# Optimization experiments

Measured on AMD Instinct MI355X. Metric: run time of the kernel, lower is better.

## Reference

```python
import jax, jax.numpy as jnp
import numpy as np

RES = (128, 128)       # frequency modes (fx, fy)
T = (1.0, 1.0)         # period per dimension
J = 2                  # simplex dimension (polygon)
B = 2                  # batch size
NV = 512               # num vertices = num elements (polygon ring)


def setup_inputs() -> dict:
    key = jax.random.key(0)
    V = jax.random.uniform(key, (B, NV, 2), dtype=jnp.float32)
    idx = jnp.arange(NV, dtype=jnp.int32)
    # polygon ring connectivity: edge i = (i, i+1 mod NV)
    E = jnp.broadcast_to(jnp.stack([idx, (idx + 1) % NV], axis=-1)[None], (B, NV, 2))
    D = jnp.ones((B, NV, 1), jnp.float32)
    return {"V": V, "E": E, "D": D}


def _omega():
    # freq_init='fft': integer fft/rfft frequencies, scaled by 2*pi/t per dim
    f0 = np.fft.fftfreq(RES[0], d=1.0 / RES[0])
    f1 = np.fft.rfftfreq(RES[1], d=1.0 / RES[1])
    om = np.stack(np.meshgrid(f0, f1, indexing='ij'), axis=-1).astype(np.float32)
    om[..., 0] *= 2.0 * np.pi / T[0]
    om[..., 1] *= 2.0 * np.pi / T[1]
    return jnp.asarray(om)  # (fx, fy//2+1, 2)


def reference(V, E, D):
    b, nv, nd = V.shape
    # subdim: append auxiliary origin vertex, turn edges into triangles
    Vaux = jnp.concatenate([V, jnp.zeros((b, 1, nd), V.dtype)], axis=1)
    Eaux = jnp.concatenate([E, jnp.full((b, E.shape[1], 1), nv, E.dtype)], axis=-1)
    P = jax.vmap(lambda v, e: v[e])(Vaux, Eaux)           # (B, ne, j+1, 2)
    # C = j! * signed simplex content = det of edge vectors (2x2)
    Vs = P[:, :, :J, :] - P[:, :, J:J + 1, :]
    C = (Vs[:, :, 0, 0] * Vs[:, :, 1, 1] - Vs[:, :, 0, 1] * Vs[:, :, 1, 0])[..., None]  # (B, ne, 1)
    omega = _omega()
    sig = jnp.einsum('bejd,xyd->bejxy', P, omega)         # (B, ne, 3, fx, fy2)
    esig = jnp.stack([jnp.cos(sig), -jnp.sin(sig)], axis=-1)  # (B, ne, 3, fx, fy2, 2)
    # divided-difference denominator: prod over circular shifts 1..j
    d1 = sig - sig[:, :, jnp.array([1, 2, 0])]
    d2 = sig - sig[:, :, jnp.array([2, 0, 1])]
    denom = d1 * d2
    zero = denom == 0
    tmp = jnp.sum(esig / jnp.where(zero, 1.0, denom)[..., None], axis=2)  # (B, ne, fx, fy2, 2)
    tmp = jnp.where(jnp.any(zero, axis=2)[..., None], 0.0, tmp)
    CD = C * D                                            # (B, ne, nch=1)
    F = jnp.einsum('bexyr,bec->bxycr', tmp, CD)           # (B, fx, fy2, 1, 2)
    # DC component: -1/j! * sum(C*D)
    dc = -jnp.sum(CD, axis=1) / 2.0                       # (B, 1)
    F = F.at[:, 0, 0].set(dc[..., None])
    F = -F                                                # img(F, deg=j=2): multiply by i^2 = -1
    F = F * (RES[0] ** J)                                 # density-preserving normalization
    return F
```

## Files before the change

kernel.cpp:

```cpp
#include <hip/hip_runtime.h>
#include <math.h>


#define NVERT 512
#define RESX  128
#define RESY2 65
#define BATCH 2
#define KXSPL 64
#define CHUNKS 8
#define ELEN  (NVERT / CHUNKS)

__device__ __forceinline__ float sig_eval(float x, float omx, float y, float omy) {
#pragma clang fp contract(off)
  float p = x * omx;
  float q = y * omy;
  return p + q;
}

extern "C" __global__ __launch_bounds__(512, 2)
void ddsl_spec(const float* __restrict__ V, const float* __restrict__ D,
               float* __restrict__ out) {
  const int lane = threadIdx.x;
  const int c    = threadIdx.y;
  const int ky   = blockIdx.x;
  const int b    = blockIdx.y;
  const int z    = blockIdx.z;

  __shared__ float2 sV[NVERT];
  __shared__ float  sCD[NVERT];
  __shared__ float  red[2][CHUNKS][KXSPL];
  __shared__ float  sDCv;

  const int tid = c * KXSPL + lane;

  {
    const float2* Vb = (const float2*)(V + b * (NVERT * 2));
    const int i = tid;
    const int j = (i + 1) & (NVERT - 1);
    float2 v0 = Vb[i];
    float2 v1 = Vb[j];
    float dv = D[b * NVERT + i];
    sV[i] = v0;
    sCD[i] = (v0.x * v1.y - v0.y * v1.x) * dv;
  }
  __syncthreads();

  const int kx = z * KXSPL + lane;
  const int kxi = (kx < 64) ? kx : kx - 128;
  const float kxf = (float)kxi;
  const float kyf = (float)ky;
  const float TWO_PI = 6.2831854820251465f;
  const float omx = TWO_PI * kxf;
  const float omy = TWO_PI * kyf;

  const int e0 = c * ELEN;

  float2 v = sV[e0];
  float s0 = sig_eval(v.x, omx, v.y, omy);
  float r0 = kxf * v.x + kyf * v.y;
  float rf0 = __builtin_amdgcn_fractf(r0);
  float c0  = __builtin_amdgcn_cosf(rf0);
  float sn0 = __builtin_amdgcn_sinf(rf0);

  float accRe = 0.0f, accIm = 0.0f;

#pragma unroll 4
  for (int e = e0; e < e0 + ELEN; ++e) {
    const int j = (e + 1) & (NVERT - 1);
    float2 v1 = sV[j];
    float cd = sCD[e];

    float s1 = sig_eval(v1.x, omx, v1.y, omy);
    float r1 = kxf * v1.x + kyf * v1.y;
    float rf1 = __builtin_amdgcn_fractf(r1);
    float c1  = __builtin_amdgcn_cosf(rf1);
    float sn1 = __builtin_amdgcn_sinf(rf1);

    float d01 = s0 - s1;
    float prod = s0 * s1 * d01;
    bool invalid = fabsf(prod) < 1e-30f;
    float cdE = invalid ? 0.0f : cd;
    float pr  = invalid ? 1.0f : prod;
    float inv = __builtin_amdgcn_rcpf(pr);

    float a0 = s1 * inv;
    float a1 = s0 * inv;
    float a2 = d01 * inv;
    float re = fmaf(c0, a0, fmaf(-c1, a1, a2));
    float im = fmaf(sn1, a1, -(sn0 * a0));

    accRe = fmaf(cdE, re, accRe);
    accIm = fmaf(cdE, im, accIm);

    s0 = s1; c0 = c1; sn0 = sn1;
  }

  red[0][c][lane] = accRe;
  red[1][c][lane] = accIm;
  __syncthreads();

  float val = 0.0f;
  if (c < 2) {
    float s = 0.0f;
#pragma unroll
    for (int k = 0; k < CHUNKS; ++k) s += red[c][k][lane];
    val = -16384.0f * s;
  } else if (c == 2 && ky == 0 && z == 0) {
    float s = 0.0f;
#pragma unroll
    for (int k = 0; k < NVERT / 64; ++k) s += sCD[lane + 64 * k];
    for (int off = 32; off > 0; off >>= 1) s += __shfl_down(s, off, 64);
    if (lane == 0) sDCv = 8192.0f * s;
  }
  __syncthreads();

  if (c < 2) {
    if (ky == 0 && z == 0 && lane == 0) val = sDCv;
    out[b * (RESX * RESY2 * 2) + kx * (RESY2 * 2) + ky * 2 + c] = val;
  }
}

extern "C" void kernel_launch(void* const* d_in, const int* in_sizes, int n_in,
                              void* d_out, int out_size, void* d_ws, size_t ws_size,
                              hipStream_t stream) {
  (void)in_sizes; (void)n_in; (void)d_ws; (void)ws_size; (void)out_size;
  const float* V = (const float*)d_in[0];
  const float* D = (const float*)d_in[2];
  float* out = (float*)d_out;

  dim3 grid(RESY2, BATCH, 2);
  dim3 block(KXSPL, CHUNKS, 1);
  ddsl_spec<<<grid, block, 0, stream>>>(V, D, out);
}
```

Measured before the change: 68.77 us.

## Repartition kx/edge work into smaller blocks and vectorize edge loop in pairs

Changes the block shape from 64 kx by 8 edge chunks to 16 kx by 16 edge chunks, and raises the grid depth from 2 to 8, so there are more, smaller blocks (256 threads) to spread over the GPU. The edge loop processes two edges per iteration with float2 vector types so the compiler can emit packed FP32 math. Vertices are stored as separate x and y arrays in shared memory. The phase is computed from sig times 1/(2π) instead of a separate dot product, which drops one multiply-add but can change rounding slightly. The risk is that smaller wave groups mean lanes in a wavefront read different edges, which could cause LDS bank conflicts, and each vertex block is reloaded by more blocks.

Measured after the change: 63.77 us. -7.3%, faster.

```diff
diff --git a/kernel.cpp b/kernel.cpp
--- a/kernel.cpp
+++ b/kernel.cpp
@@ -6,106 +6,118 @@
 #define RESX  128
 #define RESY2 65
 #define BATCH 2
-#define KXSPL 64
-#define CHUNKS 8
-#define ELEN  (NVERT / CHUNKS)
+#define NKX   16
+#define NCH   16
+#define ELEN  (NVERT / NCH)
 
-__device__ __forceinline__ float sig_eval(float x, float omx, float y, float omy) {
+typedef float f2 __attribute__((ext_vector_type(2)));
+
+__device__ __forceinline__ float sig1(float x, float y, float omx, float omy) {
 #pragma clang fp contract(off)
   float p = x * omx;
   float q = y * omy;
   return p + q;
 }
 
-extern "C" __global__ __launch_bounds__(512, 2)
+__device__ __forceinline__ f2 sig2(f2 x, f2 y, float omx, float omy) {
+#pragma clang fp contract(off)
+  f2 p = x * omx;
+  f2 q = y * omy;
+  return p + q;
+}
+
+extern "C" __global__ __launch_bounds__(256, 4)
 void ddsl_spec(const float* __restrict__ V, const float* __restrict__ D,
                float* __restrict__ out) {
-  const int lane = threadIdx.x;
-  const int c    = threadIdx.y;
-  const int ky   = blockIdx.x;
-  const int b    = blockIdx.y;
-  const int z    = blockIdx.z;
+  const int tx = threadIdx.x;
+  const int ty = threadIdx.y;
+  const int ky = blockIdx.x;
+  const int b  = blockIdx.y;
+  const int z  = blockIdx.z;
 
-  __shared__ float2 sV[NVERT];
-  __shared__ float  sCD[NVERT];
-  __shared__ float  red[2][CHUNKS][KXSPL];
-  __shared__ float  sDCv;
+  __shared__ float sVx[NVERT];
+  __shared__ float sVy[NVERT];
+  __shared__ __align__(8) float sCD[NVERT];
+  __shared__ float red[2][NCH][NKX];
+  __shared__ float sDCv;
 
-  const int tid = c * KXSPL + lane;
+  const int tid = ty * NKX + tx;
 
   {
     const float2* Vb = (const float2*)(V + b * (NVERT * 2));
-    const int i = tid;
-    const int j = (i + 1) & (NVERT - 1);
-    float2 v0 = Vb[i];
-    float2 v1 = Vb[j];
-    float dv = D[b * NVERT + i];
-    sV[i] = v0;
-    sCD[i] = (v0.x * v1.y - v0.y * v1.x) * dv;
+    for (int i = tid; i < NVERT; i += 256) {
+      const int j = (i + 1) & (NVERT - 1);
+      float2 v0 = Vb[i];
+      float2 v1 = Vb[j];
+      sVx[i] = v0.x;
+      sVy[i] = v0.y;
+      sCD[i] = (v0.x * v1.y - v0.y * v1.x) * D[b * NVERT + i];
+    }
   }
   __syncthreads();
 
-  const int kx = z * KXSPL + lane;
-  const int kxi = (kx < 64) ? kx : kx - 128;
-  const float kxf = (float)kxi;
+  const int kx = z * NKX + tx;
+  const float kxf = (float)((kx < 64) ? kx : kx - 128);
   const float kyf = (float)ky;
   const float TWO_PI = 6.2831854820251465f;
+  const float INV2PI = 0.15915493667125702f;
   const float omx = TWO_PI * kxf;
   const float omy = TWO_PI * kyf;
 
-  const int e0 = c * ELEN;
+  const int e0 = ty * ELEN;
 
-  float2 v = sV[e0];
-  float s0 = sig_eval(v.x, omx, v.y, omy);
-  float r0 = kxf * v.x + kyf * v.y;
-  float rf0 = __builtin_amdgcn_fractf(r0);
-  float c0  = __builtin_amdgcn_cosf(rf0);
-  float sn0 = __builtin_amdgcn_sinf(rf0);
+  float sP = sig1(sVx[e0], sVy[e0], omx, omy);
+  float rfP = __builtin_amdgcn_fractf(sP * INV2PI);
+  float cP  = __builtin_amdgcn_cosf(rfP);
+  float snP = __builtin_amdgcn_sinf(rfP);
 
-  float accRe = 0.0f, accIm = 0.0f;
+  f2 accRe = {0.0f, 0.0f};
+  f2 accIm = {0.0f, 0.0f};
 
 #pragma unroll 4
-  for (int e = e0; e < e0 + ELEN; ++e) {
-    const int j = (e + 1) & (NVERT - 1);
-    float2 v1 = sV[j];
-    float cd = sCD[e];
+  for (int t = 0; t < ELEN / 2; ++t) {
+    const int e = e0 + 2 * t;
+    const int j1 = (e + 1) & (NVERT - 1);
+    const int j2 = (e + 2) & (NVERT - 1);
+    f2 xx = {sVx[j1], sVx[j2]};
+    f2 yy = {sVy[j1], sVy[j2]};
+    f2 cd = *(const f2*)&sCD[e];
 
-    float s1 = sig_eval(v1.x, omx, v1.y, omy);
-    float r1 = kxf * v1.x + kyf * v1.y;
-    float rf1 = __builtin_amdgcn_fractf(r1);
-    float c1  = __builtin_amdgcn_cosf(rf1);
-    float sn1 = __builtin_amdgcn_sinf(rf1);
+    f2 sN = sig2(xx, yy, omx, omy);
+    f2 rf = sN * INV2PI;
+    float rf0 = __builtin_amdgcn_fractf(rf.x);
+    float rf1 = __builtin_amdgcn_fractf(rf.y);
+    f2 cN  = {__builtin_amdgcn_cosf(rf0), __builtin_amdgcn_cosf(rf1)};
+    f2 snN = {__builtin_amdgcn_sinf(rf0), __builtin_amdgcn_sinf(rf1)};
 
-    float d01 = s0 - s1;
-    float prod = s0 * s1 * d01;
-    bool invalid = fabsf(prod) < 1e-30f;
-    float cdE = invalid ? 0.0f : cd;
-    float pr  = invalid ? 1.0f : prod;
-    float inv = __builtin_amdgcn_rcpf(pr);
+    f2 s0  = {sP, sN.x};
+    f2 c0  = {cP, cN.x};
+    f2 sn0 = {snP, snN.x};
+    f2 d01 = s0 - sN;
+    f2 prod = s0 * sN * d01;
+    float i0 = (fabsf(prod.x) < 1e-30f) ? 0.0f : __builtin_amdgcn_rcpf(prod.x);
+    float i1 = (fabsf(prod.y) < 1e-30f) ? 0.0f : __builtin_amdgcn_rcpf(prod.y);
+    f2 inv = {i0, i1};
 
-    float a0 = s1 * inv;
-    float a1 = s0 * inv;
-    float a2 = d01 * inv;
-    float re = fmaf(c0, a0, fmaf(-c1, a1, a2));
-    float im = fmaf(sn1, a1, -(sn0 * a0));
+    f2 a0 = sN * inv;
+    f2 a1 = s0 * inv;
+    f2 a2 = d01 * inv;
+    f2 re = __builtin_elementwise_fma(c0, a0,
+            __builtin_elementwise_fma(-cN, a1, a2));
+    f2 im = __builtin_elementwise_fma(snN, a1, -(sn0 * a0));
 
-    accRe = fmaf(cdE, re, accRe);
-    accIm = fmaf(cdE, im, accIm);
+    accRe = __builtin_elementwise_fma(cd, re, accRe);
+    accIm = __builtin_elementwise_fma(cd, im, accIm);
 
-    s0 = s1; c0 = c1; sn0 = sn1;
+    sP = sN.y; cP = cN.y; snP = snN.y;
   }
 
-  red[0][c][lane] = accRe;
-  red[1][c][lane] = accIm;
+  red[0][ty][tx] = accRe.x + accRe.y;
+  red[1][ty][tx] = accIm.x + accIm.y;
   __syncthreads();
 
-  float val = 0.0f;
-  if (c < 2) {
-    float s = 0.0f;
-#pragma unroll
-    for (int k = 0; k < CHUNKS; ++k) s += red[c][k][lane];
-    val = -16384.0f * s;
-  } else if (c == 2 && ky == 0 && z == 0) {
+  if (ky == 0 && z == 0 && tid >= 128 && tid < 192) {
+    const int lane = tid - 128;
     float s = 0.0f;
 #pragma unroll
     for (int k = 0; k < NVERT / 64; ++k) s += sCD[lane + 64 * k];
@@ -114,9 +126,13 @@
   }
   __syncthreads();
 
-  if (c < 2) {
-    if (ky == 0 && z == 0 && lane == 0) val = sDCv;
-    out[b * (RESX * RESY2 * 2) + kx * (RESY2 * 2) + ky * 2 + c] = val;
+  if (ty < 2) {
+    float s = 0.0f;
+#pragma unroll
+    for (int k = 0; k < NCH; ++k) s += red[ty][k][tx];
+    float val = -16384.0f * s;
+    if (ky == 0 && z == 0 && tx == 0) val = sDCv;
+    out[b * (RESX * RESY2 * 2) + kx * (RESY2 * 2) + ky * 2 + ty] = val;
   }
 }
 
@@ -128,7 +144,7 @@
   const float* D = (const float*)d_in[2];
   float* out = (float*)d_out;
 
-  dim3 grid(RESY2, BATCH, 2);
-  dim3 block(KXSPL, CHUNKS, 1);
+  dim3 grid(RESY2, BATCH, 8);
+  dim3 block(NKX, NCH, 1);
   ddsl_spec<<<grid, block, 0, stream>>>(V, D, out);
 }
```
